# Kernel optimization log

Measured on AMD Instinct MI355X. Metric: run time of the kernel, lower is better.

## Reference

```python
import jax, jax.numpy as jnp
import numpy as np

B, N, H, W = 2, 2048, 256, 256
C = 128
STATE = 256
FEAT_IN = C + 2
MID = 6  # layer_num - 2 residual blocks
OUT_DIM = 2


def setup_inputs() -> dict:
    key = jax.random.key(0)
    ks = jax.random.split(key, 8)
    s = 0.01  # matches nn.Linear init normal_(0.0, 0.01)
    features = jax.random.normal(ks[0], (B, C, H, W), jnp.float32)
    base_point = jax.random.uniform(ks[1], (B, N, 2), dtype=jnp.float32)
    adj = jax.random.uniform(ks[2], (B, N, N), dtype=jnp.float32) / N  # row-normalized-ish adjacency
    point_mask = jnp.ones((B, 1, N, 1), jnp.float32)
    w_first = jax.random.normal(ks[3], (2, FEAT_IN, STATE), jnp.float32) * s  # fc1, fc2
    b_first = jnp.zeros((2, STATE), jnp.float32)
    w_mid = jax.random.normal(ks[4], (MID, 4, STATE, STATE), jnp.float32) * s  # per block: gcn1.fc1, gcn1.fc2, gcn2.fc1, gcn2.fc2
    b_mid = jnp.zeros((MID, 4, STATE), jnp.float32)
    w_last = jax.random.normal(ks[5], (2, STATE, STATE), jnp.float32) * s
    b_last = jnp.zeros((2, STATE), jnp.float32)
    w_fc = jax.random.normal(ks[6], (STATE, OUT_DIM), jnp.float32) * s
    b_fc = jnp.zeros((OUT_DIM,), jnp.float32)
    return dict(features=features, base_point=base_point, adj=adj, point_mask=point_mask,
                w_first=w_first, b_first=b_first, w_mid=w_mid, b_mid=b_mid,
                w_last=w_last, b_last=b_last, w_fc=w_fc, b_fc=b_fc)


def _interp(feat, coords, h, w):
    # feat: [B, H*W, C]; coords: [B, N, 2] in [0,1] (x, y order as in torch code)
    Xs = coords[:, :, 0] * w
    Ys = coords[:, :, 1] * h
    X0f = jnp.floor(Xs); X1f = X0f + 1.0
    Y0f = jnp.floor(Ys); Y1f = Y0f + 1.0
    w00 = (X1f - Xs) * (Y1f - Ys)
    w01 = (X1f - Xs) * (Ys - Y0f)
    w10 = (Xs - X0f) * (Y1f - Ys)
    w11 = (Xs - X0f) * (Ys - Y0f)
    X0 = jnp.clip(X0f, 0, w - 1).astype(jnp.int32)
    X1 = jnp.clip(X1f, 0, w - 1).astype(jnp.int32)
    Y0 = jnp.clip(Y0f, 0, h - 1).astype(jnp.int32)
    Y1 = jnp.clip(Y1f, 0, h - 1).astype(jnp.int32)
    def gather(idx):  # idx: [B, N] -> [B, N, C]
        return jnp.take_along_axis(feat, idx[:, :, None], axis=1)
    m00 = gather(X0 + Y0 * w)
    m01 = gather(X0 + Y1 * w)
    m10 = gather(X1 + Y0 * w)
    m11 = gather(X1 + Y1 * w)
    return (w00[..., None] * m00 + w01[..., None] * m01 +
            w10[..., None] * m10 + w11[..., None] * m11)


def _gconv(x, adj, w1, b1, w2, b2):
    # GraphConvolution: fc1(x) + fc2(adj @ x)
    return (x @ w1 + b1) + (jnp.matmul(adj, x) @ w2 + b2)


def _res_block(x, adj, w, b):
    h = jax.nn.relu(_gconv(x, adj, w[0], b[0], w[1], b[1]))
    h = _gconv(h, adj, w[2], b[2], w[3], b[3])
    return jax.nn.relu(h + x)


def _forward(features, base_point, adj, point_mask,
             w_first, b_first, w_mid, b_mid, w_last, b_last, w_fc, b_fc):
    b, c, h, w = features.shape
    feat_flat = features.reshape(b, c, h * w).transpose(0, 2, 1)  # [B, HW, C]
    cnn_feature = _interp(feat_flat, base_point, h, w)            # [B, N, C]
    x = jnp.concatenate([cnn_feature, base_point], axis=2)        # [B, N, C+2]
    x = _gconv(x, adj, w_first[0], b_first[0], w_first[1], b_first[1])
    for i in range(MID):
        x = _res_block(x, adj, w_mid[i], b_mid[i])
    x = _gconv(x, adj, w_last[0], b_last[0], w_last[1], b_last[1])
    gcn_pred = x @ w_fc + b_fc                                    # [B, N, out_dim]
    mask = point_mask.squeeze(1)                                  # [B, N, 1]
    pred_points = base_point + gcn_pred[:, :, :2] * mask
    lap1 = base_point - jnp.matmul(adj, base_point)
    lap2 = pred_points - jnp.matmul(adj, pred_points)
    lap_energy = jnp.sqrt((((lap2 - lap1) ** 2) + 1e-10).sum(-1)).mean(-1)  # [B]
    return pred_points, gcn_pred, lap_energy


def reference(features, base_point, adj, point_mask,
              w_first, b_first, w_mid, b_mid, w_last, b_last, w_fc, b_fc):
    return _forward(features, base_point, adj, point_mask,
                    w_first, b_first, w_mid, b_mid, w_last, b_last, w_fc, b_fc)
```

## Files before the change

kernel.cpp:

```cpp
#include <hip/hip_runtime.h>
#include <hip/hip_bf16.h>
#include <math.h>

#define BB 2
#define NN 2048
#define HH 256
#define WW 256
#define CC 128
#define MIDN 6
#define YSTR 1048576

typedef __hip_bfloat16 bf16;
typedef short short8 __attribute__((ext_vector_type(8)));
typedef float f32x4 __attribute__((ext_vector_type(4)));
typedef unsigned short ushort4v __attribute__((ext_vector_type(4)));

__device__ inline float bf2f(unsigned short u) {
    return __uint_as_float(((unsigned int)u) << 16);
}
__device__ inline unsigned short f2bf_bits(float f) {
    __hip_bfloat16 h = __float2bfloat16(f);
    return *reinterpret_cast<unsigned short*>(&h);
}

__global__ void prep_kernel(const float* __restrict__ adj, bf16* __restrict__ adjB,
                            const float* __restrict__ features, const float* __restrict__ base_point,
                            bf16* __restrict__ x0p,
                            const float* __restrict__ w_first, const float* __restrict__ w_mid,
                            const float* __restrict__ w_last, bf16* __restrict__ wT) {
    __shared__ float tbuf[32][33];
    int bid = blockIdx.x;
    int t = threadIdx.x;
    if (bid < 1024) {
        int wv = t >> 6, lane = t & 63;
        int idx = bid * 4 + wv;
        int b   = idx >> 11;
        float bx = base_point[idx * 2 + 0];
        float by = base_point[idx * 2 + 1];
        float xs = bx * (float)WW;
        float ys = by * (float)HH;
        float x0f = floorf(xs), y0f = floorf(ys);
        float x1f = x0f + 1.f, y1f = y0f + 1.f;
        float w00 = (x1f - xs) * (y1f - ys);
        float w01 = (x1f - xs) * (ys - y0f);
        float w10 = (xs - x0f) * (y1f - ys);
        float w11 = (xs - x0f) * (ys - y0f);
        int X0 = (int)fminf(fmaxf(x0f, 0.f), (float)(WW - 1));
        int X1 = (int)fminf(fmaxf(x1f, 0.f), (float)(WW - 1));
        int Y0 = (int)fminf(fmaxf(y0f, 0.f), (float)(HH - 1));
        int Y1 = (int)fminf(fmaxf(y1f, 0.f), (float)(HH - 1));
        int p00 = Y0 * WW + X0, p01 = Y1 * WW + X0;
        int p10 = Y0 * WW + X1, p11 = Y1 * WW + X1;
        int c0 = lane * 2;
        const float* f0 = features + (size_t)(b * CC + c0) * (HH * WW);
        const float* f1 = f0 + HH * WW;
        float v0 = w00 * f0[p00] + w01 * f0[p01] + w10 * f0[p10] + w11 * f0[p11];
        float v1 = w00 * f1[p00] + w01 * f1[p01] + w10 * f1[p10] + w11 * f1[p11];
        unsigned int pk = (unsigned int)f2bf_bits(v0) | ((unsigned int)f2bf_bits(v1) << 16);
        *(unsigned int*)(x0p + (size_t)idx * 256 + c0) = pk;
        unsigned int pk2 = 0;
        if (lane == 0)
            pk2 = (unsigned int)f2bf_bits(bx) | ((unsigned int)f2bf_bits(by) << 16);
        *(unsigned int*)(x0p + (size_t)idx * 256 + 128 + c0) = pk2;
    } else if (bid < 2048) {
        int sub = bid - 1024;
        size_t i = ((size_t)sub * 8192) + (size_t)t * 32;
        #pragma unroll
        for (int h = 0; h < 4; ++h) {
            float4 f0 = *(const float4*)(adj + i + h * 8);
            float4 f1 = *(const float4*)(adj + i + h * 8 + 4);
            short8 v;
            v[0] = (short)f2bf_bits(f0.x); v[1] = (short)f2bf_bits(f0.y);
            v[2] = (short)f2bf_bits(f0.z); v[3] = (short)f2bf_bits(f0.w);
            v[4] = (short)f2bf_bits(f1.x); v[5] = (short)f2bf_bits(f1.y);
            v[6] = (short)f2bf_bits(f1.z); v[7] = (short)f2bf_bits(f1.w);
            *(short8*)(adjB + i + h * 8) = v;
        }
    } else {
        int idx = bid - 2048;
        int m   = idx >> 6;
        int sub = idx & 63;
        int bx = sub & 7, by = sub >> 3;
        const float* S; int R;
        if (m < 2)       { S = w_first + (size_t)m * 130 * 256; R = 130; }
        else if (m < 26) { S = w_mid + (size_t)(m - 2) * 65536; R = 256; }
        else             { S = w_last + (size_t)(m - 26) * 65536; R = 256; }
        bf16* D = wT + (size_t)m * 65536;
        int tx = t & 31, ty = t >> 5;
        int c0 = bx * 32, r0 = by * 32;
        #pragma unroll
        for (int k = 0; k < 4; ++k) {
            int r = r0 + ty + 8 * k;
            tbuf[ty + 8 * k][tx] = (r < R) ? S[(size_t)r * 256 + c0 + tx] : 0.f;
        }
        __syncthreads();
        #pragma unroll
        for (int k = 0; k < 4; ++k) {
            int c = c0 + ty + 8 * k;
            D[(size_t)c * 256 + r0 + tx] = __float2bfloat16(tbuf[tx][ty + 8 * k]);
        }
    }
}

__global__ __launch_bounds__(256, 2) void s_kernel(const bf16* __restrict__ gprev,
                                                   const bf16* __restrict__ Yb,
                                                   const float* __restrict__ bias1,
                                                   const float* __restrict__ bias2,
                                                   const bf16* __restrict__ res,
                                                   int relu,
                                                   const bf16* __restrict__ wcat,
                                                   bf16* __restrict__ xR,
                                                   bf16* __restrict__ g1out,
                                                   bf16* __restrict__ g2T) {
    __shared__ char lds[81920];
    char* Bl = lds;
    char* Al = lds + 65536;
    int tid = threadIdx.x;
    int bid = blockIdx.x;
    int lin = (bid & 7) * 64 + (bid >> 3);
    int ct = lin & 3, rt = lin >> 2;
    int lane = tid & 63, w = tid >> 6;
    int wr = w >> 1, wc = w & 1;
    int row16 = lane & 15, kg = lane >> 4;

    #pragma unroll
    for (int rnd = 0; rnd < 16; ++rnd) {
        int plane = rnd >> 2;
        int dp = (rnd & 3) * 4096 + tid * 16;
        int row = dp >> 7;
        int cb = dp & 127;
        int sc = (cb ^ ((row & 7) << 4)) >> 1;
        __builtin_amdgcn_global_load_lds(
            (const __attribute__((address_space(1))) void*)(wcat + (size_t)(ct * 128 + row) * 256 + plane * 64 + sc),
            (__attribute__((address_space(3))) void*)(Bl + plane * 16384 + (rnd & 3) * 4096 + (w << 10)),
            16, 0, 0);
    }

    {
        int arow = tid >> 3;
        int acb  = (tid * 16) & 127;
        int ridx = rt * 32 + arow;
        int awb  = arow * 128 + (acb ^ ((arow & 7) << 4));
        #pragma unroll
        for (int rnd = 0; rnd < 4; ++rnd) {
            int gcol = rnd * 64 + (acb >> 1);
            size_t off = (size_t)ridx * 256 + gcol;
            short8 pk;
            if (Yb) {
                short8 gv  = *(const short8*)(gprev + off);
                short8 y0v = *(const short8*)(Yb + off);
                short8 y1v = *(const short8*)(Yb + YSTR + off);
                short8 y2v = *(const short8*)(Yb + 2 * YSTR + off);
                short8 y3v = *(const short8*)(Yb + 3 * YSTR + off);
                short8 rv = {};
                if (res) rv = *(const short8*)(res + off);
                #pragma unroll
                for (int j = 0; j < 8; ++j) {
                    float f = bf2f((unsigned short)gv[j]) + bf2f((unsigned short)y0v[j])
                            + bf2f((unsigned short)y1v[j]) + bf2f((unsigned short)y2v[j])
                            + bf2f((unsigned short)y3v[j])
                            + bias1[gcol + j] + bias2[gcol + j];
                    if (res)  f += bf2f((unsigned short)rv[j]);
                    if (relu) f = fmaxf(f, 0.f);
                    pk[j] = (short)f2bf_bits(f);
                }
            } else {
                pk = *(const short8*)(gprev + off);
            }
            if (ct == 0) *(short8*)(xR + off) = pk;
            *(short8*)(Al + rnd * 4096 + awb) = pk;
        }
    }

    asm volatile("s_waitcnt vmcnt(0) lgkmcnt(0)" ::: "memory");
    __builtin_amdgcn_s_barrier();

    f32x4 acc[4] = {};
    int arow = wr * 16 + row16;
    #pragma unroll
    for (int kk = 0; kk < 8; ++kk) {
        int plane = kk >> 1, kk2 = kk & 1;
        int kof = kk2 * 64 + kg * 16;
        short8 a = *(const short8*)(Al + plane * 4096 + arow * 128 + (kof ^ ((arow & 7) << 4)));
        #pragma unroll
        for (int nf = 0; nf < 4; ++nf) {
            int fr = wc * 64 + nf * 16 + row16;
            short8 bfr = *(const short8*)(Bl + plane * 16384 + fr * 128 + (kof ^ ((fr & 7) << 4)));
            acc[nf] = __builtin_amdgcn_mfma_f32_16x16x32_bf16(a, bfr, acc[nf], 0, 0, 0);
        }
    }

    int cbase = ct * 128 + wc * 64;
    int rb = rt * 32 + wr * 16 + kg * 4;
    if (cbase < 256) {
        #pragma unroll
        for (int nf = 0; nf < 4; ++nf) {
            int c = cbase + nf * 16 + row16;
            #pragma unroll
            for (int j = 0; j < 4; ++j)
                *reinterpret_cast<unsigned short*>(&g1out[(size_t)(rb + j) * 256 + c]) = f2bf_bits(acc[nf][j]);
        }
    } else {
        #pragma unroll
        for (int nf = 0; nf < 4; ++nf) {
            int c = cbase - 256 + nf * 16 + row16;
            ushort4v pk;
            #pragma unroll
            for (int j = 0; j < 4; ++j) pk[j] = f2bf_bits(acc[nf][j]);
            *(ushort4v*)(g2T + (size_t)c * 4096 + rb) = pk;
        }
    }
}

__global__ __launch_bounds__(256, 2) void adjb_kernel(const bf16* __restrict__ adjB,
                                                      const bf16* __restrict__ g2T,
                                                      bf16* __restrict__ Ybase) {
    __shared__ char lds[73728];
    int tid = threadIdx.x;
    int bid = blockIdx.x;
    int lin = (bid & 7) * 64 + (bid >> 3);
    int ct = lin & 3, rt = (lin >> 2) & 15, z = lin >> 6;
    int b = z >> 2, ks = z & 3;
    const bf16* Aadj = adjB + (size_t)b * NN * NN + (size_t)(rt * 128) * NN + ks * 512;
    const bf16* Bg   = g2T + (size_t)(ct * 64) * 4096 + b * NN + ks * 512;
    bf16* Yo = Ybase + (size_t)ks * YSTR;
    int lane = tid & 63, w = tid >> 6;
    int wr = w >> 1, wc = w & 1;
    int row16 = lane & 15, kg = lane >> 4;
    f32x4 acc[4][2] = {};

    #define STAGE(BUF, IT)                                                                \
        {                                                                                 \
            int k0 = (IT) * 64;                                                           \
            _Pragma("unroll")                                                             \
            for (int rnd = 0; rnd < 4; ++rnd) {                                           \
                int d = tid * 16 + rnd * 4096;                                            \
                int row = d >> 7, cb = d & 127;                                           \
                int sc = (cb ^ ((row & 7) << 4)) >> 1;                                    \
                __builtin_amdgcn_global_load_lds(                                         \
                    (const __attribute__((address_space(1))) void*)(Aadj + (size_t)row * NN + k0 + sc), \
                    (__attribute__((address_space(3))) void*)(lds + (BUF) * 24576 + rnd * 4096 + (w << 10)), \
                    16, 0, 0);                                                            \
            }                                                                             \
            _Pragma("unroll")                                                             \
            for (int rnd = 0; rnd < 2; ++rnd) {                                           \
                int d = tid * 16 + rnd * 4096;                                            \
                int row = d >> 7, cb = d & 127;                                           \
                int sc = (cb ^ ((row & 7) << 4)) >> 1;                                    \
                __builtin_amdgcn_global_load_lds(                                         \
                    (const __attribute__((address_space(1))) void*)(Bg + (size_t)row * 4096 + k0 + sc), \
                    (__attribute__((address_space(3))) void*)(lds + (BUF) * 24576 + 16384 + rnd * 4096 + (w << 10)), \
                    16, 0, 0);                                                            \
            }                                                                             \
        }

    #define MFMA_STEP(BUF)                                                                \
        _Pragma("unroll")                                                                 \
        for (int kk = 0; kk < 2; ++kk) {                                                  \
            short8 a[4], bfr[2];                                                          \
            _Pragma("unroll")                                                             \
            for (int mf = 0; mf < 4; ++mf) {                                              \
                int row = wr * 64 + mf * 16 + row16;                                      \
                a[mf] = *(const short8*)(lds + (BUF) * 24576 + row * 128 +                \
                          (((kk * 64) + kg * 16) ^ ((row & 7) << 4)));                    \
            }                                                                             \
            _Pragma("unroll")                                                             \
            for (int nf = 0; nf < 2; ++nf) {                                              \
                int fr = wc * 32 + nf * 16 + row16;                                       \
                bfr[nf] = *(const short8*)(lds + (BUF) * 24576 + 16384 + fr * 128 +       \
                          (((kk * 64) + kg * 16) ^ ((fr & 7) << 4)));                     \
            }                                                                             \
            _Pragma("unroll")                                                             \
            for (int mf = 0; mf < 4; ++mf)                                                \
                _Pragma("unroll")                                                         \
                for (int nf = 0; nf < 2; ++nf)                                            \
                    acc[mf][nf] = __builtin_amdgcn_mfma_f32_16x16x32_bf16(a[mf], bfr[nf], acc[mf][nf], 0, 0, 0); \
        }

    #define ADJB_ITER(BUF, SBUF, DOSTAGE, CNT)                                            \
        if (DOSTAGE) { STAGE(SBUF, SIT); }                                                \
        asm volatile("s_waitcnt vmcnt(" #CNT ")" ::: "memory");                           \
        __builtin_amdgcn_s_barrier();                                                     \
        MFMA_STEP(BUF);                                                                   \
        __builtin_amdgcn_s_barrier();

    STAGE(0, 0);
    STAGE(1, 1);
    { enum { SIT = 2 }; ADJB_ITER(0, 2, 1, 12) }
    { enum { SIT = 3 }; ADJB_ITER(1, 0, 1, 12) }
    { enum { SIT = 4 }; ADJB_ITER(2, 1, 1, 12) }
    { enum { SIT = 5 }; ADJB_ITER(0, 2, 1, 12) }
    { enum { SIT = 6 }; ADJB_ITER(1, 0, 1, 12) }
    { enum { SIT = 7 }; ADJB_ITER(2, 1, 1, 12) }
    { enum { SIT = 0 }; ADJB_ITER(0, 0, 0, 6) }
    { enum { SIT = 0 }; ADJB_ITER(1, 0, 0, 0) }

    #pragma unroll
    for (int mf = 0; mf < 4; ++mf) {
        #pragma unroll
        for (int nf = 0; nf < 2; ++nf) {
            int c  = ct * 64 + wc * 32 + nf * 16 + row16;
            int r0 = b * NN + rt * 128 + wr * 64 + mf * 16 + kg * 4;
            #pragma unroll
            for (int j = 0; j < 4; ++j)
                *reinterpret_cast<unsigned short*>(&Yo[(size_t)(r0 + j) * 256 + c]) = f2bf_bits(acc[mf][nf][j]);
        }
    }
    #undef STAGE
    #undef MFMA_STEP
    #undef ADJB_ITER
}

__global__ void head_kernel(const bf16* __restrict__ g1, const bf16* __restrict__ Yb,
                            const float* __restrict__ b_last,
                            const float* __restrict__ w_fc, const float* __restrict__ b_fc,
                            const float* __restrict__ base_point, const float* __restrict__ point_mask,
                            float* __restrict__ out, float* __restrict__ dpts) {
    if (blockIdx.x == 0 && threadIdx.x < 2)
        out[4 * BB * NN + threadIdx.x] = 0.f;
    int row = blockIdx.x * 256 + threadIdx.x;
    float s0 = b_fc[0], s1 = b_fc[1];
    for (int d = 0; d < 256; d += 8) {
        size_t off = (size_t)row * 256 + d;
        short8 a = *(const short8*)(g1 + off);
        float zv[8];
        #pragma unroll
        for (int j = 0; j < 8; ++j) zv[j] = bf2f((unsigned short)a[j]);
        #pragma unroll
        for (int p = 0; p < 4; ++p) {
            short8 yv = *(const short8*)(Yb + (size_t)p * YSTR + off);
            #pragma unroll
            for (int j = 0; j < 8; ++j) zv[j] += bf2f((unsigned short)yv[j]);
        }
        #pragma unroll
        for (int j = 0; j < 8; ++j) {
            float z = zv[j] + b_last[d + j] + b_last[256 + d + j];
            s0 += z * w_fc[(d + j) * 2 + 0];
            s1 += z * w_fc[(d + j) * 2 + 1];
        }
    }
    float m  = point_mask[row];
    float p0 = base_point[row * 2 + 0] + s0 * m;
    float p1 = base_point[row * 2 + 1] + s1 * m;
    out[row * 2 + 0] = p0;
    out[row * 2 + 1] = p1;
    out[2 * BB * NN + row * 2 + 0] = s0;
    out[2 * BB * NN + row * 2 + 1] = s1;
    dpts[row * 2 + 0] = s0 * m;
    dpts[row * 2 + 1] = s1 * m;
}

__global__ void lap_rows(const bf16* __restrict__ adjB, const float* __restrict__ dpts,
                         float* __restrict__ outlap) {
    __shared__ float sd[4];
    int w    = threadIdx.x >> 6;
    int lane = threadIdx.x & 63;
    int row  = blockIdx.x * 4 + w;
    int b = row >> 11, n = row & 2047;
    const bf16* ar = adjB + (size_t)b * NN * NN + (size_t)n * NN;
    const float* db = dpts + (size_t)b * NN * 2;
    float s0 = 0.f, s1 = 0.f;
    for (int k4 = 0; k4 < 4; ++k4) {
        int k = k4 * 512 + lane * 8;
        short8 av = *(const short8*)(ar + k);
        #pragma unroll
        for (int j = 0; j < 8; ++j) {
            float a = bf2f((unsigned short)av[j]);
            float2 dv = *(const float2*)(db + (k + j) * 2);
            s0 += a * dv.x;
            s1 += a * dv.y;
        }
    }
    for (int off = 32; off; off >>= 1) {
        s0 += __shfl_xor(s0, off);
        s1 += __shfl_xor(s1, off);
    }
    if (lane == 0) {
        float e0 = dpts[(size_t)row * 2 + 0] - s0;
        float e1 = dpts[(size_t)row * 2 + 1] - s1;
        sd[w] = sqrtf(e0 * e0 + e1 * e1 + 1e-10f);
    }
    __syncthreads();
    if (threadIdx.x == 0) {
        float s = (sd[0] + sd[1] + sd[2] + sd[3]) * (1.f / (float)NN);
        atomicAdd(&outlap[b], s);
    }
}

extern "C" void kernel_launch(void* const* d_in, const int* in_sizes, int n_in,
                              void* d_out, int out_size, void* d_ws, size_t ws_size,
                              hipStream_t stream) {
    const float* features   = (const float*)d_in[0];
    const float* base_point = (const float*)d_in[1];
    const float* adj        = (const float*)d_in[2];
    const float* point_mask = (const float*)d_in[3];
    const float* w_first    = (const float*)d_in[4];
    const float* b_first    = (const float*)d_in[5];
    const float* w_mid      = (const float*)d_in[6];
    const float* b_mid      = (const float*)d_in[7];
    const float* w_last     = (const float*)d_in[8];
    const float* b_last     = (const float*)d_in[9];
    const float* w_fc       = (const float*)d_in[10];
    const float* b_fc       = (const float*)d_in[11];
    float* out = (float*)d_out;
    char* W = (char*)d_ws;

    bf16* adjB   = (bf16*)W;
    bf16* wT     = (bf16*)(W + 16777216);
    bf16* x0p    = (bf16*)(W + 20447232);
    bf16* g1b[2] = { (bf16*)(W + 22544384), (bf16*)(W + 24641536) };
    bf16* g2T    = (bf16*)(W + 26738688);
    bf16* Yb     = (bf16*)(W + 28835840);
    bf16* xsl[2] = { (bf16*)(W + 37224448), (bf16*)(W + 39321600) };
    bf16* xscr   = (bf16*)(W + 41418752);
    float* dpts  = (float*)(W + 43515904);

    prep_kernel<<<3840, 256, 0, stream>>>(adj, adjB, features, base_point, x0p,
                                          w_first, w_mid, w_last, wT);

    s_kernel<<<512, 256, 0, stream>>>(x0p, nullptr, nullptr, nullptr, nullptr, 0,
                                      wT, xscr, g1b[0], g2T);
    adjb_kernel<<<512, 256, 0, stream>>>(adjB, g2T, Yb);

    for (int k = 1; k < 14; ++k) {
        const float *bb1, *bb2;
        const bf16* resp = nullptr;
        bf16* xw;
        int rl;
        if (k == 1) {
            bb1 = b_first; bb2 = b_first + 256; rl = 0; xw = xsl[0];
        } else if ((k & 1) == 0) {
            int m = (k - 2) / 2;
            bb1 = b_mid + (size_t)m * 1024; bb2 = bb1 + 256;
            rl = 1; xw = xscr;
        } else {
            int m = (k - 3) / 2;
            bb1 = b_mid + (size_t)m * 1024 + 512; bb2 = bb1 + 256;
            rl = 1;
            resp = xsl[m & 1];
            xw   = xsl[((k - 1) / 2) & 1];
        }
        s_kernel<<<512, 256, 0, stream>>>(g1b[(k - 1) & 1], Yb, bb1, bb2, resp, rl,
                                          wT + (size_t)2 * k * 65536, xw, g1b[k & 1], g2T);
        adjb_kernel<<<512, 256, 0, stream>>>(adjB, g2T, Yb);
    }

    head_kernel<<<16, 256, 0, stream>>>(g1b[1], Yb, b_last, w_fc, b_fc,
                                        base_point, point_mask, out, dpts);
    lap_rows<<<1024, 256, 0, stream>>>(adjB, dpts, out + 4 * BB * NN);
}
```

Before: 324.6 us.

## Double split-K in adjacency GEMM and split prep into separate kernels

The adjacency-times-features kernel now splits K into 8 slices of 256 instead of 4 of 512, which doubles the grid to 1024 blocks and cuts LDS to a two-buffer pipeline so more blocks can be resident. The consumer kernels (s_kernel prologue and head) now reduce 8 partial Y planes instead of 4, and the workspace layout is shifted to make room. The adj fp32-to-bf16 conversion is moved out of the combined prep kernel into its own kernel. This trades more partial-sum write and read traffic plus a shallower software pipeline for better occupancy and parallelism in the dominant GEMM.

```diff
diff --git a/kernel.cpp b/kernel.cpp
--- a/kernel.cpp
+++ b/kernel.cpp
@@ -23,8 +23,23 @@
     return *reinterpret_cast<unsigned short*>(&h);
 }
 
-__global__ void prep_kernel(const float* __restrict__ adj, bf16* __restrict__ adjB,
-                            const float* __restrict__ features, const float* __restrict__ base_point,
+__global__ __launch_bounds__(256) void conv_kernel(const float* __restrict__ adj,
+                                                   bf16* __restrict__ adjB) {
+    size_t base = ((size_t)blockIdx.x * 256 + threadIdx.x) * 16;
+    #pragma unroll
+    for (int h = 0; h < 2; ++h) {
+        float4 f0 = *(const float4*)(adj + base + h * 8);
+        float4 f1 = *(const float4*)(adj + base + h * 8 + 4);
+        short8 v;
+        v[0] = (short)f2bf_bits(f0.x); v[1] = (short)f2bf_bits(f0.y);
+        v[2] = (short)f2bf_bits(f0.z); v[3] = (short)f2bf_bits(f0.w);
+        v[4] = (short)f2bf_bits(f1.x); v[5] = (short)f2bf_bits(f1.y);
+        v[6] = (short)f2bf_bits(f1.z); v[7] = (short)f2bf_bits(f1.w);
+        *(short8*)(adjB + base + h * 8) = v;
+    }
+}
+
+__global__ void misc_kernel(const float* __restrict__ features, const float* __restrict__ base_point,
                             bf16* __restrict__ x0p,
                             const float* __restrict__ w_first, const float* __restrict__ w_mid,
                             const float* __restrict__ w_last, bf16* __restrict__ wT) {
@@ -62,22 +77,8 @@
         if (lane == 0)
             pk2 = (unsigned int)f2bf_bits(bx) | ((unsigned int)f2bf_bits(by) << 16);
         *(unsigned int*)(x0p + (size_t)idx * 256 + 128 + c0) = pk2;
-    } else if (bid < 2048) {
-        int sub = bid - 1024;
-        size_t i = ((size_t)sub * 8192) + (size_t)t * 32;
-        #pragma unroll
-        for (int h = 0; h < 4; ++h) {
-            float4 f0 = *(const float4*)(adj + i + h * 8);
-            float4 f1 = *(const float4*)(adj + i + h * 8 + 4);
-            short8 v;
-            v[0] = (short)f2bf_bits(f0.x); v[1] = (short)f2bf_bits(f0.y);
-            v[2] = (short)f2bf_bits(f0.z); v[3] = (short)f2bf_bits(f0.w);
-            v[4] = (short)f2bf_bits(f1.x); v[5] = (short)f2bf_bits(f1.y);
-            v[6] = (short)f2bf_bits(f1.z); v[7] = (short)f2bf_bits(f1.w);
-            *(short8*)(adjB + i + h * 8) = v;
-        }
     } else {
-        int idx = bid - 2048;
+        int idx = bid - 1024;
         int m   = idx >> 6;
         int sub = idx & 63;
         int bx = sub & 7, by = sub >> 3;
@@ -148,18 +149,20 @@
             short8 pk;
             if (Yb) {
                 short8 gv  = *(const short8*)(gprev + off);
-                short8 y0v = *(const short8*)(Yb + off);
-                short8 y1v = *(const short8*)(Yb + YSTR + off);
-                short8 y2v = *(const short8*)(Yb + 2 * YSTR + off);
-                short8 y3v = *(const short8*)(Yb + 3 * YSTR + off);
+                float fv[8];
+                #pragma unroll
+                for (int j = 0; j < 8; ++j) fv[j] = bf2f((unsigned short)gv[j]);
+                #pragma unroll
+                for (int p = 0; p < 8; ++p) {
+                    short8 yv = *(const short8*)(Yb + (size_t)p * YSTR + off);
+                    #pragma unroll
+                    for (int j = 0; j < 8; ++j) fv[j] += bf2f((unsigned short)yv[j]);
+                }
                 short8 rv = {};
                 if (res) rv = *(const short8*)(res + off);
                 #pragma unroll
                 for (int j = 0; j < 8; ++j) {
-                    float f = bf2f((unsigned short)gv[j]) + bf2f((unsigned short)y0v[j])
-                            + bf2f((unsigned short)y1v[j]) + bf2f((unsigned short)y2v[j])
-                            + bf2f((unsigned short)y3v[j])
-                            + bias1[gcol + j] + bias2[gcol + j];
+                    float f = fv[j] + bias1[gcol + j] + bias2[gcol + j];
                     if (res)  f += bf2f((unsigned short)rv[j]);
                     if (relu) f = fmaxf(f, 0.f);
                     pk[j] = (short)f2bf_bits(f);
@@ -215,14 +218,14 @@
 __global__ __launch_bounds__(256, 2) void adjb_kernel(const bf16* __restrict__ adjB,
                                                       const bf16* __restrict__ g2T,
                                                       bf16* __restrict__ Ybase) {
-    __shared__ char lds[73728];
+    __shared__ char lds[49152];
     int tid = threadIdx.x;
     int bid = blockIdx.x;
-    int lin = (bid & 7) * 64 + (bid >> 3);
+    int lin = (bid & 7) * 128 + (bid >> 3);
     int ct = lin & 3, rt = (lin >> 2) & 15, z = lin >> 6;
-    int b = z >> 2, ks = z & 3;
-    const bf16* Aadj = adjB + (size_t)b * NN * NN + (size_t)(rt * 128) * NN + ks * 512;
-    const bf16* Bg   = g2T + (size_t)(ct * 64) * 4096 + b * NN + ks * 512;
+    int b = z >> 3, ks = z & 7;
+    const bf16* Aadj = adjB + (size_t)b * NN * NN + (size_t)(rt * 128) * NN + ks * 256;
+    const bf16* Bg   = g2T + (size_t)(ct * 64) * 4096 + b * NN + ks * 256;
     bf16* Yo = Ybase + (size_t)ks * YSTR;
     int lane = tid & 63, w = tid >> 6;
     int wr = w >> 1, wc = w & 1;
@@ -277,23 +280,25 @@
                     acc[mf][nf] = __builtin_amdgcn_mfma_f32_16x16x32_bf16(a[mf], bfr[nf], acc[mf][nf], 0, 0, 0); \
         }
 
-    #define ADJB_ITER(BUF, SBUF, DOSTAGE, CNT)                                            \
-        if (DOSTAGE) { STAGE(SBUF, SIT); }                                                \
-        asm volatile("s_waitcnt vmcnt(" #CNT ")" ::: "memory");                           \
-        __builtin_amdgcn_s_barrier();                                                     \
-        MFMA_STEP(BUF);                                                                   \
-        __builtin_amdgcn_s_barrier();
-
     STAGE(0, 0);
     STAGE(1, 1);
-    { enum { SIT = 2 }; ADJB_ITER(0, 2, 1, 12) }
-    { enum { SIT = 3 }; ADJB_ITER(1, 0, 1, 12) }
-    { enum { SIT = 4 }; ADJB_ITER(2, 1, 1, 12) }
-    { enum { SIT = 5 }; ADJB_ITER(0, 2, 1, 12) }
-    { enum { SIT = 6 }; ADJB_ITER(1, 0, 1, 12) }
-    { enum { SIT = 7 }; ADJB_ITER(2, 1, 1, 12) }
-    { enum { SIT = 0 }; ADJB_ITER(0, 0, 0, 6) }
-    { enum { SIT = 0 }; ADJB_ITER(1, 0, 0, 0) }
+    asm volatile("s_waitcnt vmcnt(6)" ::: "memory");
+    __builtin_amdgcn_s_barrier();
+    MFMA_STEP(0);
+    __builtin_amdgcn_s_barrier();
+    STAGE(0, 2);
+    asm volatile("s_waitcnt vmcnt(6)" ::: "memory");
+    __builtin_amdgcn_s_barrier();
+    MFMA_STEP(1);
+    __builtin_amdgcn_s_barrier();
+    STAGE(1, 3);
+    asm volatile("s_waitcnt vmcnt(6)" ::: "memory");
+    __builtin_amdgcn_s_barrier();
+    MFMA_STEP(0);
+    __builtin_amdgcn_s_barrier();
+    asm volatile("s_waitcnt vmcnt(0)" ::: "memory");
+    __builtin_amdgcn_s_barrier();
+    MFMA_STEP(1);
 
     #pragma unroll
     for (int mf = 0; mf < 4; ++mf) {
@@ -308,7 +313,6 @@
     }
     #undef STAGE
     #undef MFMA_STEP
-    #undef ADJB_ITER
 }
 
 __global__ void head_kernel(const bf16* __restrict__ g1, const bf16* __restrict__ Yb,
@@ -327,7 +331,7 @@
         #pragma unroll
         for (int j = 0; j < 8; ++j) zv[j] = bf2f((unsigned short)a[j]);
         #pragma unroll
-        for (int p = 0; p < 4; ++p) {
+        for (int p = 0; p < 8; ++p) {
             short8 yv = *(const short8*)(Yb + (size_t)p * YSTR + off);
             #pragma unroll
             for (int j = 0; j < 8; ++j) zv[j] += bf2f((unsigned short)yv[j]);
@@ -411,16 +415,17 @@
     bf16* g1b[2] = { (bf16*)(W + 22544384), (bf16*)(W + 24641536) };
     bf16* g2T    = (bf16*)(W + 26738688);
     bf16* Yb     = (bf16*)(W + 28835840);
-    bf16* xsl[2] = { (bf16*)(W + 37224448), (bf16*)(W + 39321600) };
-    bf16* xscr   = (bf16*)(W + 41418752);
-    float* dpts  = (float*)(W + 43515904);
-
-    prep_kernel<<<3840, 256, 0, stream>>>(adj, adjB, features, base_point, x0p,
+    bf16* xsl[2] = { (bf16*)(W + 45613056), (bf16*)(W + 47710208) };
+    bf16* xscr   = (bf16*)(W + 49807360);
+    float* dpts  = (float*)(W + 51904512);
+
+    conv_kernel<<<2048, 256, 0, stream>>>(adj, adjB);
+    misc_kernel<<<2816, 256, 0, stream>>>(features, base_point, x0p,
                                           w_first, w_mid, w_last, wT);
 
     s_kernel<<<512, 256, 0, stream>>>(x0p, nullptr, nullptr, nullptr, nullptr, 0,
                                       wT, xscr, g1b[0], g2T);
-    adjb_kernel<<<512, 256, 0, stream>>>(adjB, g2T, Yb);
+    adjb_kernel<<<1024, 256, 0, stream>>>(adjB, g2T, Yb);
 
     for (int k = 1; k < 14; ++k) {
         const float *bb1, *bb2;
@@ -442,7 +447,7 @@
         }
         s_kernel<<<512, 256, 0, stream>>>(g1b[(k - 1) & 1], Yb, bb1, bb2, resp, rl,
                                           wT + (size_t)2 * k * 65536, xw, g1b[k & 1], g2T);
-        adjb_kernel<<<512, 256, 0, stream>>>(adjB, g2T, Yb);
+        adjb_kernel<<<1024, 256, 0, stream>>>(adjB, g2T, Yb);
     }
 
     head_kernel<<<16, 256, 0, stream>>>(g1b[1], Yb, b_last, w_fc, b_fc,
```

Result: slower. 381.2 us (+17.4%).
